# Kernel tuning notes

Measured on AMD Instinct MI355X. Metric: run time of the kernel, lower is better.

## Reference

```python
import jax, jax.numpy as jnp
import numpy as np

H = 8  # heads
EPS = 1e-5


def adaln(x, t, W, b):
    # AdaLayerNorm: emb = Linear(t); scale, shift = chunk(emb, 2, dim=-1)
    emb = t @ W + b                      # [B,1,2*D]
    scale, shift = jnp.split(emb, 2, axis=-1)
    mu = jnp.mean(x, axis=-1, keepdims=True)
    var = jnp.var(x, axis=-1, keepdims=True)
    xn = (x - mu) / jnp.sqrt(var + EPS)  # elementwise_affine=False
    return xn * (1.0 + scale) + shift


def attention(x, ctx, Wq, Wk, Wv, Wo, bo):
    B, N, D = x.shape
    d = D // H
    q = (x @ Wq).reshape(B, N, H, d).transpose(0, 2, 1, 3)          # [B,H,N,d]
    k = (ctx @ Wk).reshape(B, ctx.shape[1], H, d).transpose(0, 2, 1, 3)
    v = (ctx @ Wv).reshape(B, ctx.shape[1], H, d).transpose(0, 2, 1, 3)
    sim = jnp.einsum('bhid,bhjd->bhij', q, k) * (d ** -0.5)
    attn = jax.nn.softmax(sim, axis=-1)
    out = jnp.einsum('bhij,bhjd->bhid', attn, v)
    out = out.transpose(0, 2, 1, 3).reshape(B, N, D)
    return out @ Wo + bo


def geglu_ff(x, W1, b1, W2, b2):
    u, g = jnp.split(x @ W1 + b1, 2, axis=-1)
    return (u * jax.nn.gelu(g, approximate=False)) @ W2 + b2


def setup_inputs() -> dict:
    key = jax.random.key(0)
    ks = jax.random.split(key, 16)
    D = 512
    s = 0.02
    inp = {
        'x': jax.random.normal(ks[0], (2, 2048, D), jnp.float32),
        't': jax.random.normal(ks[1], (2, 1, D), jnp.float32),
        'cond': jax.random.normal(ks[2], (2, 1024, D), jnp.float32),
        'n1_w': jax.random.normal(ks[3], (D, 2 * D), jnp.float32) * s,
        'n1_b': jnp.zeros((2 * D,), jnp.float32),
        'n2_w': jax.random.normal(ks[4], (D, 2 * D), jnp.float32) * s,
        'n2_b': jnp.zeros((2 * D,), jnp.float32),
        'n4_w': jax.random.normal(ks[5], (D, 2 * D), jnp.float32) * s,
        'n4_b': jnp.zeros((2 * D,), jnp.float32),
        'a1_q': jax.random.normal(ks[6], (D, D), jnp.float32) * s,
        'a1_k': jax.random.normal(ks[7], (D, D), jnp.float32) * s,
        'a1_v': jax.random.normal(ks[8], (D, D), jnp.float32) * s,
        'a1_o': jax.random.normal(ks[9], (D, D), jnp.float32) * s,
        'a1_ob': jnp.zeros((D,), jnp.float32),
        'a2_q': jax.random.normal(ks[10], (D, D), jnp.float32) * s,
        'a2_k': jax.random.normal(ks[11], (D, D), jnp.float32) * s,
        'a2_v': jax.random.normal(ks[12], (D, D), jnp.float32) * s,
        'a2_o': jax.random.normal(ks[13], (D, D), jnp.float32) * s,
        'a2_ob': jnp.zeros((D,), jnp.float32),
        'ff_w1': jax.random.normal(ks[14], (D, 8 * D), jnp.float32) * s,
        'ff_b1': jnp.zeros((8 * D,), jnp.float32),
        'ff_w2': jax.random.normal(ks[15], (4 * D, D), jnp.float32) * s,
        'ff_b2': jnp.zeros((D,), jnp.float32),
    }
    return inp


def reference(x, t, cond, n1_w, n1_b, n2_w, n2_b, n4_w, n4_b,
              a1_q, a1_k, a1_v, a1_o, a1_ob,
              a2_q, a2_k, a2_v, a2_o, a2_ob,
              ff_w1, ff_b1, ff_w2, ff_b2):
    # BasicTransformerBlock, is_deform=False, withT=False, inference (dropout/droppath = identity, LayerScale = identity since init_values=0)
    h = adaln(x, t, n1_w, n1_b)
    x = attention(h, h, a1_q, a1_k, a1_v, a1_o, a1_ob) + x
    h = adaln(x, t, n2_w, n2_b)
    x = attention(h, cond, a2_q, a2_k, a2_v, a2_o, a2_ob) + x
    h = adaln(x, t, n4_w, n4_b)
    x = geglu_ff(h, ff_w1, ff_b1, ff_w2, ff_b2) + x
    return x
```

## Files before the change

kernel.cpp:

```cpp
#include <hip/hip_runtime.h>
#include <math.h>

#define D_MODEL 512
#define NHEADS  8
#define DHEAD   64

typedef __bf16  bf16x2 __attribute__((ext_vector_type(2)));
typedef __bf16  bf16x4 __attribute__((ext_vector_type(4)));
typedef __bf16  bf16x8 __attribute__((ext_vector_type(8)));
typedef float   f32x4  __attribute__((ext_vector_type(4)));

#define QSCALE 0.18033688f
#define DEFER_THR 11.5416f

__device__ __forceinline__ void gload16(const __bf16* g, __bf16* l) {
    __builtin_amdgcn_global_load_lds(
        (const __attribute__((address_space(1))) unsigned int*)g,
        (__attribute__((address_space(3))) unsigned int*)l, 16, 0, 0);
}

__device__ __forceinline__ void transpose_tile(
        const float* __restrict__ src, __bf16* __restrict__ dst,
        int K, int N, int k0, int n0) {
    __shared__ float t[64][65];
    int tid = threadIdx.x;
    int r = tid >> 6, c = tid & 63;
#pragma unroll
    for (int i = 0; i < 16; ++i)
        t[r + 4 * i][c] = src[(size_t)(k0 + r + 4 * i) * N + n0 + c];
    __syncthreads();
#pragma unroll
    for (int i = 0; i < 16; ++i)
        dst[(size_t)(n0 + r + 4 * i) * K + k0 + c] = (__bf16)t[c][r + 4 * i];
}

struct PrepArgs {
    const float *t, *n1w, *n1b, *n2w, *n2b, *n4w, *n4b;
    float* emb;
    const float* ws[8]; __bf16* wd[8];
    const float *ffw1, *ffw2;
    __bf16 *ff1t, *ff2t;
    const float* cond; __bf16* cbf;
    int B, condN;
};

__global__ __launch_bounds__(256) void prep_kernel(PrepArgs a) {
    int bb = blockIdx.x, tid = threadIdx.x;
    if (bb < 24) {
        int gI = bb * 256 + tid;
        int per = a.B * 2 * D_MODEL;
        if (gI >= 3 * per) return;
        int norm = gI / per;
        int rem  = gI - norm * per;
        int b = rem / (2 * D_MODEL);
        int c = rem % (2 * D_MODEL);
        const float* W  = (norm == 0) ? a.n1w : (norm == 1 ? a.n2w : a.n4w);
        const float* bb_= (norm == 0) ? a.n1b : (norm == 1 ? a.n2b : a.n4b);
        const float* trow = a.t + (size_t)b * D_MODEL;
        float acc = bb_[c];
        for (int k = 0; k < D_MODEL; ++k)
            acc = fmaf(trow[k], W[(size_t)k * (2 * D_MODEL) + c], acc);
        a.emb[gI] = acc;
    } else if (bb < 536) {
        int w = (bb - 24) >> 6, tI = (bb - 24) & 63;
        transpose_tile(a.ws[w], a.wd[w], 512, 512, (tI >> 3) << 6, (tI & 7) << 6);
    } else if (bb < 1048) {
        int tI = bb - 536;
        transpose_tile(a.ffw1, a.ff1t, 512, 4096, (tI & 7) << 6, (tI >> 3) << 6);
    } else if (bb < 1304) {
        int tI = bb - 1048;
        transpose_tile(a.ffw2, a.ff2t, 2048, 512, (tI >> 3) << 6, (tI & 7) << 6);
    } else {
        int i = ((bb - 1304) * 256 + tid) * 4;
        if (i >= a.condN) return;
        float4 v = *(const float4*)(a.cond + i);
        bf16x2 p0, p1;
        p0[0] = (__bf16)v.x; p0[1] = (__bf16)v.y;
        p1[0] = (__bf16)v.z; p1[1] = (__bf16)v.w;
        *(bf16x2*)(a.cbf + i)     = p0;
        *(bf16x2*)(a.cbf + i + 2) = p1;
    }
}

__global__ __launch_bounds__(256) void adaln_apply_kernel(
        const float* __restrict__ x, const float* __restrict__ emb_n,
        __bf16* __restrict__ h, int N) {
    int row = blockIdx.x;
    int b = row / N;
    const float* xr = x + (size_t)row * D_MODEL;
    int tid = threadIdx.x;
    float2 v = *(const float2*)(xr + 2 * tid);
    float s = v.x + v.y, sq = v.x * v.x + v.y * v.y;
#pragma unroll
    for (int off = 32; off; off >>= 1) {
        s  += __shfl_xor(s, off);
        sq += __shfl_xor(sq, off);
    }
    __shared__ float rs[4], rq[4];
    if ((tid & 63) == 0) { rs[tid >> 6] = s; rq[tid >> 6] = sq; }
    __syncthreads();
    float tot  = rs[0] + rs[1] + rs[2] + rs[3];
    float totq = rq[0] + rq[1] + rq[2] + rq[3];
    float mu  = tot * (1.0f / D_MODEL);
    float var = totq * (1.0f / D_MODEL) - mu * mu;
    float inv = rsqrtf(var + 1e-5f);
    const float* er = emb_n + (size_t)b * (2 * D_MODEL);
    float2 sc = *(const float2*)(er + 2 * tid);
    float2 sh = *(const float2*)(er + D_MODEL + 2 * tid);
    bf16x2 o;
    o[0] = (__bf16)((v.x - mu) * inv * (1.0f + sc.x) + sh.x);
    o[1] = (__bf16)((v.y - mu) * inv * (1.0f + sc.y) + sh.y);
    *(bf16x2*)(h + (size_t)row * D_MODEL + 2 * tid) = o;
}

template<int OUT, int WM>
__device__ __forceinline__ void gemm_body(
        const __bf16* __restrict__ A, const __bf16* __restrict__ Bt,
        const float* __restrict__ bias, const float* __restrict__ res,
        void* __restrict__ Cv, int M, int K, int N, int bx, int by,
        __bf16* As, __bf16* Bs) {
    constexpr int MI = WM / 16;
    int tid = threadIdx.x;
    int wave = tid >> 6, lane = tid & 63;
    int wr = wave >> 1, wc = wave & 1;
    int r = lane & 15, g = lane >> 4;
    int rx = r & 7;
    int m0 = by * (2 * WM), n0 = bx << 6;

    int lrow = lane >> 3;
    int lcol = ((lane & 7) ^ lrow) << 3;
    const __bf16* Ag = A  + (size_t)(m0 + (wave << 3) + lrow) * K + lcol;
    const __bf16* Bg = Bt + (size_t)(n0 + (wave << 3) + lrow) * K + lcol;
    __bf16* AsW = As + (size_t)(wave << 3) * 64;
    __bf16* BsW = Bs + (size_t)(wave << 3) * 64;

    f32x4 acc[MI][2];
#pragma unroll
    for (int mi = 0; mi < MI; ++mi)
#pragma unroll
        for (int ni = 0; ni < 2; ++ni) acc[mi][ni] = (f32x4){0.f, 0.f, 0.f, 0.f};

    for (int k0 = 0; k0 < K; k0 += 64) {
        if (k0) __syncthreads();
#pragma unroll
        for (int i = 0; i < MI; ++i)
            gload16(Ag + (size_t)(i * 32) * K + k0, AsW + i * 32 * 64);
#pragma unroll
        for (int j = 0; j < 2; ++j)
            gload16(Bg + (size_t)(j * 32) * K + k0, BsW + j * 32 * 64);
        __syncthreads();
#pragma unroll
        for (int kk = 0; kk < 2; ++kk) {
            int cs = ((((kk << 2) + g) ^ rx) << 3);
            bf16x8 af[MI], bf_[2];
#pragma unroll
            for (int mi = 0; mi < MI; ++mi)
                af[mi] = *(const bf16x8*)&As[(size_t)(wr * WM + (mi << 4) + r) * 64 + cs];
#pragma unroll
            for (int ni = 0; ni < 2; ++ni)
                bf_[ni] = *(const bf16x8*)&Bs[(size_t)((wc << 5) + (ni << 4) + r) * 64 + cs];
#pragma unroll
            for (int mi = 0; mi < MI; ++mi)
#pragma unroll
                for (int ni = 0; ni < 2; ++ni)
                    acc[mi][ni] = __builtin_amdgcn_mfma_f32_16x16x32_bf16(
                        af[mi], bf_[ni], acc[mi][ni], 0, 0, 0);
        }
    }

#pragma unroll
    for (int mi = 0; mi < MI; ++mi) {
#pragma unroll
        for (int ni = 0; ni < 2; ++ni) {
            int col = n0 + (wc << 5) + (ni << 4) + r;
            float scl = (OUT == 2 && col < 512) ? QSCALE : 1.0f;
#pragma unroll
            for (int rg = 0; rg < 4; ++rg) {
                int row = m0 + wr * WM + (mi << 4) + (g << 2) + rg;
                if (OUT == 1) {
                    float v = acc[mi][ni][rg] + bias[col] + res[(size_t)row * N + col];
                    ((float*)Cv)[(size_t)row * N + col] = v;
                } else {
                    ((__bf16*)Cv)[(size_t)row * N + col] = (__bf16)(acc[mi][ni][rg] * scl);
                }
            }
        }
    }
}

template<int OUT, int WM>
__global__ __launch_bounds__(256) void gemm_bf16_kernel(
        const __bf16* __restrict__ A, const __bf16* __restrict__ Bt,
        const float* __restrict__ bias, const float* __restrict__ res,
        void* __restrict__ Cv, int M, int K, int N) {
    __shared__ __attribute__((aligned(16))) __bf16 As[2 * WM * 64];
    __shared__ __attribute__((aligned(16))) __bf16 Bs[64 * 64];
    gemm_body<OUT, WM>(A, Bt, bias, res, Cv, M, K, N, blockIdx.x, blockIdx.y, As, Bs);
}

__global__ __launch_bounds__(256) void gemm_dual_kernel(
        const __bf16* A0, const __bf16* B0, __bf16* C0, int M0,
        const __bf16* A1, const __bf16* B1, __bf16* C1, int M1) {
    __shared__ __attribute__((aligned(16))) __bf16 As[64 * 64];
    __shared__ __attribute__((aligned(16))) __bf16 Bs[64 * 64];
    int nb0 = 8 * (M0 >> 6);
    if ((int)blockIdx.x < nb0) {
        gemm_body<2, 32>(A0, B0, nullptr, nullptr, C0, M0, 512, 512,
                         blockIdx.x & 7, blockIdx.x >> 3, As, Bs);
    } else {
        int id = blockIdx.x - nb0;
        gemm_body<0, 32>(A1, B1, nullptr, nullptr, C1, M1, 512, 1024,
                         id & 15, id >> 4, As, Bs);
    }
}

__global__ __launch_bounds__(256) void gemm_geglu_bf16_kernel(
        const __bf16* __restrict__ A, const __bf16* __restrict__ W1t,
        const float* __restrict__ b1, __bf16* __restrict__ gg, int M, int K) {
    const int NOUT = 4 * D_MODEL;
    __shared__ __attribute__((aligned(16))) __bf16 AsL[128 * 64];
    __shared__ __attribute__((aligned(16))) __bf16 BuL[64 * 64];
    __shared__ __attribute__((aligned(16))) __bf16 BgL[64 * 64];
    int tid = threadIdx.x;
    int wave = tid >> 6, lane = tid & 63;
    int wr = wave >> 1, wc = wave & 1;
    int r = lane & 15, g = lane >> 4;
    int rx = r & 7;
    int m0 = blockIdx.y << 7, n0 = blockIdx.x << 6;

    int lrow = lane >> 3;
    int lcol = ((lane & 7) ^ lrow) << 3;
    const __bf16* Ag = A   + (size_t)(m0 + (wave << 3) + lrow) * K + lcol;
    const __bf16* Ug = W1t + (size_t)(n0 + (wave << 3) + lrow) * K + lcol;
    const __bf16* Gg = W1t + (size_t)(NOUT + n0 + (wave << 3) + lrow) * K + lcol;
    __bf16* AsW = AsL + (size_t)(wave << 3) * 64;
    __bf16* BuW = BuL + (size_t)(wave << 3) * 64;
    __bf16* BgW = BgL + (size_t)(wave << 3) * 64;

    f32x4 accu[4][2], accg[4][2];
#pragma unroll
    for (int mi = 0; mi < 4; ++mi)
#pragma unroll
        for (int ni = 0; ni < 2; ++ni) {
            accu[mi][ni] = (f32x4){0.f, 0.f, 0.f, 0.f};
            accg[mi][ni] = (f32x4){0.f, 0.f, 0.f, 0.f};
        }

    for (int k0 = 0; k0 < K; k0 += 64) {
        if (k0) __syncthreads();
#pragma unroll
        for (int i = 0; i < 4; ++i)
            gload16(Ag + (size_t)(i * 32) * K + k0, AsW + i * 32 * 64);
#pragma unroll
        for (int j = 0; j < 2; ++j) {
            gload16(Ug + (size_t)(j * 32) * K + k0, BuW + j * 32 * 64);
            gload16(Gg + (size_t)(j * 32) * K + k0, BgW + j * 32 * 64);
        }
        __syncthreads();
#pragma unroll
        for (int kk = 0; kk < 2; ++kk) {
            int cs = ((((kk << 2) + g) ^ rx) << 3);
            bf16x8 af[4], bu[2], bg[2];
#pragma unroll
            for (int mi = 0; mi < 4; ++mi)
                af[mi] = *(const bf16x8*)&AsL[(size_t)((wr << 6) + (mi << 4) + r) * 64 + cs];
#pragma unroll
            for (int ni = 0; ni < 2; ++ni) {
                bu[ni] = *(const bf16x8*)&BuL[(size_t)((wc << 5) + (ni << 4) + r) * 64 + cs];
                bg[ni] = *(const bf16x8*)&BgL[(size_t)((wc << 5) + (ni << 4) + r) * 64 + cs];
            }
#pragma unroll
            for (int mi = 0; mi < 4; ++mi)
#pragma unroll
                for (int ni = 0; ni < 2; ++ni) {
                    accu[mi][ni] = __builtin_amdgcn_mfma_f32_16x16x32_bf16(
                        af[mi], bu[ni], accu[mi][ni], 0, 0, 0);
                    accg[mi][ni] = __builtin_amdgcn_mfma_f32_16x16x32_bf16(
                        af[mi], bg[ni], accg[mi][ni], 0, 0, 0);
                }
        }
    }

#pragma unroll
    for (int mi = 0; mi < 4; ++mi) {
#pragma unroll
        for (int ni = 0; ni < 2; ++ni) {
            int col = n0 + (wc << 5) + (ni << 4) + r;
            float bu_ = b1[col], bg_ = b1[NOUT + col];
#pragma unroll
            for (int rg = 0; rg < 4; ++rg) {
                int row = m0 + (wr << 6) + (mi << 4) + (g << 2) + rg;
                float u  = accu[mi][ni][rg] + bu_;
                float gv = accg[mi][ni][rg] + bg_;
                float ge = 0.5f * gv * (1.0f + erff(gv * 0.70710678118654752f));
                gg[(size_t)row * NOUT + col] = (__bf16)(u * ge);
            }
        }
    }
}

__global__ __launch_bounds__(256) void attn_mfma_kernel(
        const __bf16* __restrict__ q, const __bf16* __restrict__ k,
        const __bf16* __restrict__ v, __bf16* __restrict__ o,
        int Nq, int Nk, int sq, int skv) {
    __shared__ __attribute__((aligned(16))) __bf16 Ks[2][4096];
    __shared__ __attribute__((aligned(16))) __bf16 Vt[2][4096];
    __shared__ __attribute__((aligned(16))) __bf16 Pl[4][1024];

    int tid = threadIdx.x;
    int w = tid >> 6, lane = tid & 63;
    int r = lane & 15, g = lane >> 4;
    int rx = r & 7;

    int nqb = Nq >> 6;
    int qb = blockIdx.x % nqb;
    int hh = (blockIdx.x / nqb) % NHEADS;
    int b  = blockIdx.x / (nqb * NHEADS);

    const __bf16* qp = q + ((size_t)(b * Nq + (qb << 6) + (w << 4) + r)) * sq
                         + hh * DHEAD + (g << 3);
    bf16x8 qf0 = *(const bf16x8*)qp;
    bf16x8 qf1 = *(const bf16x8*)(qp + 32);

    int krow = tid >> 2, kp_ = tid & 3;
    int va = tid & 31, vbb = tid >> 5;
    size_t kvbase = (size_t)b * Nk * skv + (size_t)hh * DHEAD;
    const __bf16* kp = k + kvbase + (size_t)krow * skv + (kp_ << 4);
    const __bf16* vp = v + kvbase + (size_t)(2 * va) * skv + (vbb << 3);
    int kwo0 = krow * 64 + ((((kp_ << 1) | 0) ^ (krow & 7)) << 3);
    int kwo1 = krow * 64 + ((((kp_ << 1) | 1) ^ (krow & 7)) << 3);
    int vwb  = vbb * 512 + ((va & 3) << 1);

    f32x4 oacc[4];
#pragma unroll
    for (int dt = 0; dt < 4; ++dt) oacc[dt] = (f32x4){0.f, 0.f, 0.f, 0.f};
    float m = -1e30f, l = 0.f;
    f32x4 saccA[4], saccB[4];
    bf16x8 kr0, kr1, vr0, vr1;
    bf16x8 vf[2][4], pa[2];

    auto LOADREG = [&](int t) {
        const __bf16* kp2 = kp + (size_t)t * 64 * skv;
        const __bf16* vp2 = vp + (size_t)t * 64 * skv;
        kr0 = *(const bf16x8*)kp2; kr1 = *(const bf16x8*)(kp2 + 8);
        vr0 = *(const bf16x8*)vp2; vr1 = *(const bf16x8*)(vp2 + skv);
    };
    auto STAGEW = [&](int buf) {
        *(bf16x8*)&Ks[buf][kwo0] = kr0;
        *(bf16x8*)&Ks[buf][kwo1] = kr1;
#pragma unroll
        for (int j = 0; j < 8; ++j) {
            bf16x2 pr; pr[0] = vr0[j]; pr[1] = vr1[j];
            *(bf16x2*)&Vt[buf][vwb + j * 64 + (((va >> 2) ^ j) << 3)] = pr;
        }
    };
    auto QKT = [&](f32x4 (&sacc)[4], int buf) {
#pragma unroll
        for (int nt = 0; nt < 4; ++nt) sacc[nt] = (f32x4){0.f, 0.f, 0.f, 0.f};
        __builtin_amdgcn_s_setprio(1);
#pragma unroll
        for (int nt = 0; nt < 4; ++nt) {
            bf16x8 kf0 = *(const bf16x8*)&Ks[buf][((nt << 4) + r) * 64 + ((g ^ rx) << 3)];
            bf16x8 kf1 = *(const bf16x8*)&Ks[buf][((nt << 4) + r) * 64 + (((g + 4) ^ rx) << 3)];
            sacc[nt] = __builtin_amdgcn_mfma_f32_16x16x32_bf16(kf0, qf0, sacc[nt], 0, 0, 0);
            sacc[nt] = __builtin_amdgcn_mfma_f32_16x16x32_bf16(kf1, qf1, sacc[nt], 0, 0, 0);
        }
        __builtin_amdgcn_s_setprio(0);
    };
    auto SMAX = [&](f32x4 (&sacc)[4]) {
        float mx = sacc[0][0];
#pragma unroll
        for (int nt = 0; nt < 4; ++nt)
#pragma unroll
            for (int rg = 0; rg < 4; ++rg) mx = fmaxf(mx, sacc[nt][rg]);
        mx = fmaxf(mx, __shfl_xor(mx, 16));
        mx = fmaxf(mx, __shfl_xor(mx, 32));
        if (!__all(mx <= m + DEFER_THR)) {
            float mn = fmaxf(m, mx);
            float al = exp2f(m - mn);
            m = mn; l *= al;
#pragma unroll
            for (int dt = 0; dt < 4; ++dt)
#pragma unroll
                for (int rg = 0; rg < 4; ++rg) oacc[dt][rg] *= al;
        }
        float sum = 0.f;
#pragma unroll
        for (int nt = 0; nt < 4; ++nt) {
            bf16x4 pk;
#pragma unroll
            for (int rg = 0; rg < 4; ++rg) {
                float p = exp2f(sacc[nt][rg] - m);
                sum += p;
                pk[rg] = (__bf16)p;
            }
            *(bf16x4*)&Pl[w][r * 64 + ((((nt << 1) | (g >> 1)) ^ rx) << 3) + ((g & 1) << 2)] = pk;
        }
        sum += __shfl_xor(sum, 16);
        sum += __shfl_xor(sum, 32);
        l += sum;
    };
    auto VFLOAD = [&](int buf) {
#pragma unroll
        for (int kh = 0; kh < 2; ++kh) {
            pa[kh] = *(const bf16x8*)&Pl[w][r * 64 + ((((kh << 2) + g) ^ rx) << 3)];
#pragma unroll
            for (int dt = 0; dt < 4; ++dt)
                vf[kh][dt] = *(const bf16x8*)&Vt[buf][((dt << 4) + r) * 64
                                                      + ((((kh << 2) + g) ^ rx) << 3)];
        }
    };
    auto PVOP = [&]() {
        __builtin_amdgcn_s_setprio(1);
#pragma unroll
        for (int kh = 0; kh < 2; ++kh)
#pragma unroll
            for (int dt = 0; dt < 4; ++dt)
                oacc[dt] = __builtin_amdgcn_mfma_f32_16x16x32_bf16(
                    vf[kh][dt], pa[kh], oacc[dt], 0, 0, 0);
        __builtin_amdgcn_s_setprio(0);
    };

    int ntiles = Nk >> 6;
    LOADREG(0);
    STAGEW(0);
    LOADREG(1);
    __syncthreads();
    QKT(saccA, 0);

    for (int t = 0; t + 1 < ntiles; t += 2) {
        STAGEW(1);
        if (t + 2 < ntiles) LOADREG(t + 2);
        SMAX(saccA);
        VFLOAD(0);
        __syncthreads();
        QKT(saccB, 1);
        PVOP();
        if (t + 2 < ntiles) {
            STAGEW(0);
            if (t + 3 < ntiles) LOADREG(t + 3);
        }
        SMAX(saccB);
        VFLOAD(1);
        __syncthreads();
        if (t + 2 < ntiles) QKT(saccA, 0);
        PVOP();
    }

    float inv = 1.0f / l;
    __bf16* ob = o + ((size_t)(b * Nq + (qb << 6) + (w << 4) + r)) * D_MODEL + hh * DHEAD;
#pragma unroll
    for (int dt = 0; dt < 4; ++dt) {
        bf16x4 ov;
#pragma unroll
        for (int rg = 0; rg < 4; ++rg) ov[rg] = (__bf16)(oacc[dt][rg] * inv);
        *(bf16x4*)&ob[(dt << 4) + (g << 2)] = ov;
    }
}

extern "C" void kernel_launch(void* const* d_in, const int* in_sizes, int n_in,
                              void* d_out, int out_size, void* d_ws, size_t ws_size,
                              hipStream_t stream) {
    const float* x    = (const float*)d_in[0];
    const float* t    = (const float*)d_in[1];
    const float* cond = (const float*)d_in[2];
    const float* n1_w = (const float*)d_in[3];
    const float* n1_b = (const float*)d_in[4];
    const float* n2_w = (const float*)d_in[5];
    const float* n2_b = (const float*)d_in[6];
    const float* n4_w = (const float*)d_in[7];
    const float* n4_b = (const float*)d_in[8];
    const float* a1_q = (const float*)d_in[9];
    const float* a1_k = (const float*)d_in[10];
    const float* a1_v = (const float*)d_in[11];
    const float* a1_o = (const float*)d_in[12];
    const float* a1_ob= (const float*)d_in[13];
    const float* a2_q = (const float*)d_in[14];
    const float* a2_k = (const float*)d_in[15];
    const float* a2_v = (const float*)d_in[16];
    const float* a2_o = (const float*)d_in[17];
    const float* a2_ob= (const float*)d_in[18];
    const float* ff_w1= (const float*)d_in[19];
    const float* ff_b1= (const float*)d_in[20];
    const float* ff_w2= (const float*)d_in[21];
    const float* ff_b2= (const float*)d_in[22];
    float* out = (float*)d_out;

    const int B  = in_sizes[1] / D_MODEL;
    const int N  = in_sizes[0] / (B * D_MODEL);
    const int Nc = in_sizes[2] / (B * D_MODEL);
    const int R  = B * N;
    const int Rc = B * Nc;

    char* Wb = (char*)d_ws;
    float* emb   = (float*)Wb;
    __bf16* r1   = (__bf16*)(Wb + 32768);
    __bf16* qkv  = r1;
    __bf16* q2   = r1;
    __bf16* kv2  = r1 + (size_t)R * 512;
    __bf16* gg   = r1;
    __bf16* h_bf = (__bf16*)(Wb + 32768 + 16777216);
    __bf16* c_bf = (__bf16*)(Wb + 32768 + 16777216 + 4194304);
    __bf16* wts  = (__bf16*)(Wb + 32768 + 16777216 + 4194304 + 2097152);
    __bf16* a1_qt = wts;
    __bf16* a1_ot = wts + 3 * 262144;
    __bf16* a2_qt = wts + 4 * 262144;
    __bf16* a2_kt = wts + 5 * 262144;
    __bf16* a2_ot = wts + 7 * 262144;
    __bf16* ff1t  = wts + 8 * 262144;
    __bf16* ff2t  = ff1t + 2097152;

    dim3 blk(256);

    PrepArgs pa;
    pa.t = t; pa.n1w = n1_w; pa.n1b = n1_b; pa.n2w = n2_w; pa.n2b = n2_b;
    pa.n4w = n4_w; pa.n4b = n4_b; pa.emb = emb;
    pa.ws[0] = a1_q; pa.ws[1] = a1_k; pa.ws[2] = a1_v; pa.ws[3] = a1_o;
    pa.ws[4] = a2_q; pa.ws[5] = a2_k; pa.ws[6] = a2_v; pa.ws[7] = a2_o;
    pa.wd[0] = a1_qt; pa.wd[1] = wts + 262144; pa.wd[2] = wts + 2 * 262144; pa.wd[3] = a1_ot;
    pa.wd[4] = a2_qt; pa.wd[5] = a2_kt; pa.wd[6] = wts + 6 * 262144; pa.wd[7] = a2_ot;
    pa.ffw1 = ff_w1; pa.ffw2 = ff_w2; pa.ff1t = ff1t; pa.ff2t = ff2t;
    pa.cond = cond; pa.cbf = c_bf; pa.B = B; pa.condN = Rc * D_MODEL;
    prep_kernel<<<dim3(1304 + (Rc * D_MODEL) / 1024), blk, 0, stream>>>(pa);

    adaln_apply_kernel<<<dim3(R), blk, 0, stream>>>(x, emb, h_bf, N);
    gemm_bf16_kernel<2, 64><<<dim3(24, R / 128), blk, 0, stream>>>(
        h_bf, a1_qt, nullptr, nullptr, qkv, R, 512, 1536);
    attn_mfma_kernel<<<dim3(B * NHEADS * (N / 64)), blk, 0, stream>>>(
        qkv, qkv + 512, qkv + 1024, h_bf, N, N, 1536, 1536);
    gemm_bf16_kernel<1, 32><<<dim3(8, R / 64), blk, 0, stream>>>(
        h_bf, a1_ot, a1_ob, x, out, R, 512, 512);

    adaln_apply_kernel<<<dim3(R), blk, 0, stream>>>(
        out, emb + (size_t)B * 2 * D_MODEL, h_bf, N);
    gemm_dual_kernel<<<dim3(8 * (R / 64) + 16 * (Rc / 64)), blk, 0, stream>>>(
        h_bf, a2_qt, q2, R, c_bf, a2_kt, kv2, Rc);
    attn_mfma_kernel<<<dim3(B * NHEADS * (N / 64)), blk, 0, stream>>>(
        q2, kv2, kv2 + 512, h_bf, N, Nc, 512, 1024);
    gemm_bf16_kernel<1, 32><<<dim3(8, R / 64), blk, 0, stream>>>(
        h_bf, a2_ot, a2_ob, out, out, R, 512, 512);

    adaln_apply_kernel<<<dim3(R), blk, 0, stream>>>(
        out, emb + (size_t)2 * B * 2 * D_MODEL, h_bf, N);
    gemm_geglu_bf16_kernel<<<dim3(32, R / 128), blk, 0, stream>>>(
        h_bf, ff1t, ff_b1, gg, R, 512);
    gemm_bf16_kernel<1, 32><<<dim3(8, R / 64), blk, 0, stream>>>(
        gg, ff2t, ff_b2, out, out, R, 2048, 512);
}
```

Before: 218.4 us.

## Load K fragments straight from global into registers, dropping K LDS staging

```diff
diff --git a/kernel.cpp b/kernel.cpp
--- a/kernel.cpp
+++ b/kernel.cpp
@@ -303,7 +303,6 @@
         const __bf16* __restrict__ q, const __bf16* __restrict__ k,
         const __bf16* __restrict__ v, __bf16* __restrict__ o,
         int Nq, int Nk, int sq, int skv) {
-    __shared__ __attribute__((aligned(16))) __bf16 Ks[2][4096];
     __shared__ __attribute__((aligned(16))) __bf16 Vt[2][4096];
     __shared__ __attribute__((aligned(16))) __bf16 Pl[4][1024];
 
@@ -322,52 +321,53 @@
     bf16x8 qf0 = *(const bf16x8*)qp;
     bf16x8 qf1 = *(const bf16x8*)(qp + 32);
 
-    int krow = tid >> 2, kp_ = tid & 3;
+    size_t kvbase = (size_t)b * Nk * skv + (size_t)hh * DHEAD;
+    const __bf16* kfb = k + kvbase + (size_t)r * skv + (g << 3);
     int va = tid & 31, vbb = tid >> 5;
-    size_t kvbase = (size_t)b * Nk * skv + (size_t)hh * DHEAD;
-    const __bf16* kp = k + kvbase + (size_t)krow * skv + (kp_ << 4);
     const __bf16* vp = v + kvbase + (size_t)(2 * va) * skv + (vbb << 3);
-    int kwo0 = krow * 64 + ((((kp_ << 1) | 0) ^ (krow & 7)) << 3);
-    int kwo1 = krow * 64 + ((((kp_ << 1) | 1) ^ (krow & 7)) << 3);
-    int vwb  = vbb * 512 + ((va & 3) << 1);
+    int vwb = vbb * 512 + ((va & 3) << 1);
 
     f32x4 oacc[4];
 #pragma unroll
     for (int dt = 0; dt < 4; ++dt) oacc[dt] = (f32x4){0.f, 0.f, 0.f, 0.f};
     float m = -1e30f, l = 0.f;
-    f32x4 saccA[4], saccB[4];
-    bf16x8 kr0, kr1, vr0, vr1;
+    bf16x8 kfA[4][2], kfB[4][2];
+    bf16x8 vr0, vr1;
     bf16x8 vf[2][4], pa[2];
-
-    auto LOADREG = [&](int t) {
-        const __bf16* kp2 = kp + (size_t)t * 64 * skv;
+    f32x4 sacc[4];
+
+    auto KLOAD = [&](bf16x8 (&kf)[4][2], int t) {
+        const __bf16* kp2 = kfb + (size_t)t * 64 * skv;
+#pragma unroll
+        for (int nt = 0; nt < 4; ++nt)
+#pragma unroll
+            for (int kh = 0; kh < 2; ++kh)
+                kf[nt][kh] = *(const bf16x8*)(kp2 + (size_t)(nt * 16) * skv + kh * 32);
+    };
+    auto VLOAD = [&](int t) {
         const __bf16* vp2 = vp + (size_t)t * 64 * skv;
-        kr0 = *(const bf16x8*)kp2; kr1 = *(const bf16x8*)(kp2 + 8);
-        vr0 = *(const bf16x8*)vp2; vr1 = *(const bf16x8*)(vp2 + skv);
+        vr0 = *(const bf16x8*)vp2;
+        vr1 = *(const bf16x8*)(vp2 + skv);
     };
     auto STAGEW = [&](int buf) {
-        *(bf16x8*)&Ks[buf][kwo0] = kr0;
-        *(bf16x8*)&Ks[buf][kwo1] = kr1;
 #pragma unroll
         for (int j = 0; j < 8; ++j) {
             bf16x2 pr; pr[0] = vr0[j]; pr[1] = vr1[j];
             *(bf16x2*)&Vt[buf][vwb + j * 64 + (((va >> 2) ^ j) << 3)] = pr;
         }
     };
-    auto QKT = [&](f32x4 (&sacc)[4], int buf) {
+    auto QKT = [&](bf16x8 (&kf)[4][2]) {
 #pragma unroll
         for (int nt = 0; nt < 4; ++nt) sacc[nt] = (f32x4){0.f, 0.f, 0.f, 0.f};
         __builtin_amdgcn_s_setprio(1);
 #pragma unroll
         for (int nt = 0; nt < 4; ++nt) {
-            bf16x8 kf0 = *(const bf16x8*)&Ks[buf][((nt << 4) + r) * 64 + ((g ^ rx) << 3)];
-            bf16x8 kf1 = *(const bf16x8*)&Ks[buf][((nt << 4) + r) * 64 + (((g + 4) ^ rx) << 3)];
-            sacc[nt] = __builtin_amdgcn_mfma_f32_16x16x32_bf16(kf0, qf0, sacc[nt], 0, 0, 0);
-            sacc[nt] = __builtin_amdgcn_mfma_f32_16x16x32_bf16(kf1, qf1, sacc[nt], 0, 0, 0);
+            sacc[nt] = __builtin_amdgcn_mfma_f32_16x16x32_bf16(kf[nt][0], qf0, sacc[nt], 0, 0, 0);
+            sacc[nt] = __builtin_amdgcn_mfma_f32_16x16x32_bf16(kf[nt][1], qf1, sacc[nt], 0, 0, 0);
         }
         __builtin_amdgcn_s_setprio(0);
     };
-    auto SMAX = [&](f32x4 (&sacc)[4]) {
+    auto SMAX = [&]() {
         float mx = sacc[0][0];
 #pragma unroll
         for (int nt = 0; nt < 4; ++nt)
@@ -396,8 +396,6 @@
             }
             *(bf16x4*)&Pl[w][r * 64 + ((((nt << 1) | (g >> 1)) ^ rx) << 3) + ((g & 1) << 2)] = pk;
         }
-        sum += __shfl_xor(sum, 16);
-        sum += __shfl_xor(sum, 32);
         l += sum;
     };
     auto VFLOAD = [&](int buf) {
@@ -422,31 +420,33 @@
     };
 
     int ntiles = Nk >> 6;
-    LOADREG(0);
+    VLOAD(0);
     STAGEW(0);
-    LOADREG(1);
+    KLOAD(kfA, 0);
+    KLOAD(kfB, 1);
+    VLOAD(1);
     __syncthreads();
-    QKT(saccA, 0);
-
-    for (int t = 0; t + 1 < ntiles; t += 2) {
-        STAGEW(1);
-        if (t + 2 < ntiles) LOADREG(t + 2);
-        SMAX(saccA);
+
+    for (int t = 0; t < ntiles; t += 2) {
+        QKT(kfA);
+        if (t + 1 < ntiles) STAGEW(1);
+        if (t + 2 < ntiles) { KLOAD(kfA, t + 2); VLOAD(t + 2); }
+        SMAX();
         VFLOAD(0);
+        PVOP();
         __syncthreads();
-        QKT(saccB, 1);
+        if (t + 1 >= ntiles) break;
+        QKT(kfB);
+        if (t + 2 < ntiles) STAGEW(0);
+        if (t + 3 < ntiles) { KLOAD(kfB, t + 3); VLOAD(t + 3); }
+        SMAX();
+        VFLOAD(1);
         PVOP();
-        if (t + 2 < ntiles) {
-            STAGEW(0);
-            if (t + 3 < ntiles) LOADREG(t + 3);
-        }
-        SMAX(saccB);
-        VFLOAD(1);
         __syncthreads();
-        if (t + 2 < ntiles) QKT(saccA, 0);
-        PVOP();
-    }
-
+    }
+
+    l += __shfl_xor(l, 16);
+    l += __shfl_xor(l, 32);
     float inv = 1.0f / l;
     __bf16* ob = o + ((size_t)(b * Nq + (qb << 6) + (w << 4) + r)) * D_MODEL + hh * DHEAD;
 #pragma unroll
```

After: 265.5 us. +21.6%, slower.

## Double attention query tile to 128 rows with 8 waves sharing K/V staging

Applied to the files above, without the earlier changes.

```diff
diff --git a/kernel.cpp b/kernel.cpp
--- a/kernel.cpp
+++ b/kernel.cpp
@@ -299,31 +299,33 @@
     }
 }
 
-__global__ __launch_bounds__(256) void attn_mfma_kernel(
+__global__ __launch_bounds__(512) void attn_mfma_kernel(
         const __bf16* __restrict__ q, const __bf16* __restrict__ k,
         const __bf16* __restrict__ v, __bf16* __restrict__ o,
         int Nq, int Nk, int sq, int skv) {
     __shared__ __attribute__((aligned(16))) __bf16 Ks[2][4096];
     __shared__ __attribute__((aligned(16))) __bf16 Vt[2][4096];
-    __shared__ __attribute__((aligned(16))) __bf16 Pl[4][1024];
+    __shared__ __attribute__((aligned(16))) __bf16 Pl[8][1024];
 
     int tid = threadIdx.x;
     int w = tid >> 6, lane = tid & 63;
     int r = lane & 15, g = lane >> 4;
     int rx = r & 7;
 
-    int nqb = Nq >> 6;
+    int nqb = Nq >> 7;
     int qb = blockIdx.x % nqb;
     int hh = (blockIdx.x / nqb) % NHEADS;
     int b  = blockIdx.x / (nqb * NHEADS);
 
-    const __bf16* qp = q + ((size_t)(b * Nq + (qb << 6) + (w << 4) + r)) * sq
+    const __bf16* qp = q + ((size_t)(b * Nq + (qb << 7) + (w << 4) + r)) * sq
                          + hh * DHEAD + (g << 3);
     bf16x8 qf0 = *(const bf16x8*)qp;
     bf16x8 qf1 = *(const bf16x8*)(qp + 32);
 
-    int krow = tid >> 2, kp_ = tid & 3;
-    int va = tid & 31, vbb = tid >> 5;
+    bool isK = (tid >= 256);
+    int sidx = tid & 255;
+    int krow = sidx >> 2, kp_ = sidx & 3;
+    int va = sidx & 31, vbb = sidx >> 5;
     size_t kvbase = (size_t)b * Nk * skv + (size_t)hh * DHEAD;
     const __bf16* kp = k + kvbase + (size_t)krow * skv + (kp_ << 4);
     const __bf16* vp = v + kvbase + (size_t)(2 * va) * skv + (vbb << 3);
@@ -336,22 +338,28 @@
     for (int dt = 0; dt < 4; ++dt) oacc[dt] = (f32x4){0.f, 0.f, 0.f, 0.f};
     float m = -1e30f, l = 0.f;
     f32x4 saccA[4], saccB[4];
-    bf16x8 kr0, kr1, vr0, vr1;
+    bf16x8 sr0, sr1;
     bf16x8 vf[2][4], pa[2];
 
     auto LOADREG = [&](int t) {
-        const __bf16* kp2 = kp + (size_t)t * 64 * skv;
-        const __bf16* vp2 = vp + (size_t)t * 64 * skv;
-        kr0 = *(const bf16x8*)kp2; kr1 = *(const bf16x8*)(kp2 + 8);
-        vr0 = *(const bf16x8*)vp2; vr1 = *(const bf16x8*)(vp2 + skv);
+        if (isK) {
+            const __bf16* kp2 = kp + (size_t)t * 64 * skv;
+            sr0 = *(const bf16x8*)kp2; sr1 = *(const bf16x8*)(kp2 + 8);
+        } else {
+            const __bf16* vp2 = vp + (size_t)t * 64 * skv;
+            sr0 = *(const bf16x8*)vp2; sr1 = *(const bf16x8*)(vp2 + skv);
+        }
     };
     auto STAGEW = [&](int buf) {
-        *(bf16x8*)&Ks[buf][kwo0] = kr0;
-        *(bf16x8*)&Ks[buf][kwo1] = kr1;
-#pragma unroll
-        for (int j = 0; j < 8; ++j) {
-            bf16x2 pr; pr[0] = vr0[j]; pr[1] = vr1[j];
-            *(bf16x2*)&Vt[buf][vwb + j * 64 + (((va >> 2) ^ j) << 3)] = pr;
+        if (isK) {
+            *(bf16x8*)&Ks[buf][kwo0] = sr0;
+            *(bf16x8*)&Ks[buf][kwo1] = sr1;
+        } else {
+#pragma unroll
+            for (int j = 0; j < 8; ++j) {
+                bf16x2 pr; pr[0] = sr0[j]; pr[1] = sr1[j];
+                *(bf16x2*)&Vt[buf][vwb + j * 64 + (((va >> 2) ^ j) << 3)] = pr;
+            }
         }
     };
     auto QKT = [&](f32x4 (&sacc)[4], int buf) {
@@ -396,8 +404,6 @@
             }
             *(bf16x4*)&Pl[w][r * 64 + ((((nt << 1) | (g >> 1)) ^ rx) << 3) + ((g & 1) << 2)] = pk;
         }
-        sum += __shfl_xor(sum, 16);
-        sum += __shfl_xor(sum, 32);
         l += sum;
     };
     auto VFLOAD = [&](int buf) {
@@ -447,8 +453,10 @@
         PVOP();
     }
 
+    l += __shfl_xor(l, 16);
+    l += __shfl_xor(l, 32);
     float inv = 1.0f / l;
-    __bf16* ob = o + ((size_t)(b * Nq + (qb << 6) + (w << 4) + r)) * D_MODEL + hh * DHEAD;
+    __bf16* ob = o + ((size_t)(b * Nq + (qb << 7) + (w << 4) + r)) * D_MODEL + hh * DHEAD;
 #pragma unroll
     for (int dt = 0; dt < 4; ++dt) {
         bf16x4 ov;
@@ -526,7 +534,7 @@
     adaln_apply_kernel<<<dim3(R), blk, 0, stream>>>(x, emb, h_bf, N);
     gemm_bf16_kernel<2, 64><<<dim3(24, R / 128), blk, 0, stream>>>(
         h_bf, a1_qt, nullptr, nullptr, qkv, R, 512, 1536);
-    attn_mfma_kernel<<<dim3(B * NHEADS * (N / 64)), blk, 0, stream>>>(
+    attn_mfma_kernel<<<dim3(B * NHEADS * (N / 128)), dim3(512), 0, stream>>>(
         qkv, qkv + 512, qkv + 1024, h_bf, N, N, 1536, 1536);
     gemm_bf16_kernel<1, 32><<<dim3(8, R / 64), blk, 0, stream>>>(
         h_bf, a1_ot, a1_ob, x, out, R, 512, 512);
@@ -535,7 +543,7 @@
         out, emb + (size_t)B * 2 * D_MODEL, h_bf, N);
     gemm_dual_kernel<<<dim3(8 * (R / 64) + 16 * (Rc / 64)), blk, 0, stream>>>(
         h_bf, a2_qt, q2, R, c_bf, a2_kt, kv2, Rc);
-    attn_mfma_kernel<<<dim3(B * NHEADS * (N / 64)), blk, 0, stream>>>(
+    attn_mfma_kernel<<<dim3(B * NHEADS * (N / 128)), dim3(512), 0, stream>>>(
         q2, kv2, kv2 + 512, h_bf, N, Nc, 512, 1024);
     gemm_bf16_kernel<1, 32><<<dim3(8, R / 64), blk, 0, stream>>>(
         h_bf, a2_ot, a2_ob, out, out, R, 512, 512);
```

After: 211.3 us, median of 2. 3.2% less time.

## Switch attention to 32x32x16 MFMA with 128-query blocks and XCD-aware block mapping

Applied to the files above, without the earlier changes.

```diff
diff --git a/kernel.cpp b/kernel.cpp
--- a/kernel.cpp
+++ b/kernel.cpp
@@ -9,6 +9,7 @@
 typedef __bf16  bf16x4 __attribute__((ext_vector_type(4)));
 typedef __bf16  bf16x8 __attribute__((ext_vector_type(8)));
 typedef float   f32x4  __attribute__((ext_vector_type(4)));
+typedef float   f32x16 __attribute__((ext_vector_type(16)));
 
 #define QSCALE 0.18033688f
 #define DEFER_THR 11.5416f
@@ -305,22 +306,29 @@
         int Nq, int Nk, int sq, int skv) {
     __shared__ __attribute__((aligned(16))) __bf16 Ks[2][4096];
     __shared__ __attribute__((aligned(16))) __bf16 Vt[2][4096];
-    __shared__ __attribute__((aligned(16))) __bf16 Pl[4][1024];
+    __shared__ __attribute__((aligned(16))) __bf16 Pl[4][2048];
 
     int tid = threadIdx.x;
     int w = tid >> 6, lane = tid & 63;
-    int r = lane & 15, g = lane >> 4;
-    int rx = r & 7;
-
-    int nqb = Nq >> 6;
-    int qb = blockIdx.x % nqb;
-    int hh = (blockIdx.x / nqb) % NHEADS;
-    int b  = blockIdx.x / (nqb * NHEADS);
-
-    const __bf16* qp = q + ((size_t)(b * Nq + (qb << 6) + (w << 4) + r)) * sq
-                         + hh * DHEAD + (g << 3);
-    bf16x8 qf0 = *(const bf16x8*)qp;
-    bf16x8 qf1 = *(const bf16x8*)(qp + 32);
+    int c = lane & 31;
+    int hg = lane >> 5;
+    int cx = c & 7;
+
+    int nwg = gridDim.x;
+    int cpx = nwg >> 3;
+    int bid = (int)blockIdx.x;
+    int lb  = (bid & 7) * cpx + (bid >> 3);
+
+    int nqb = Nq >> 7;
+    int qb = lb % nqb;
+    int hh = (lb / nqb) % NHEADS;
+    int b  = lb / (nqb * NHEADS);
+
+    const __bf16* qp = q + ((size_t)(b * Nq + (qb << 7) + (w << 5) + c)) * sq
+                         + hh * DHEAD + (hg << 3);
+    bf16x8 qf[4];
+#pragma unroll
+    for (int ks = 0; ks < 4; ++ks) qf[ks] = *(const bf16x8*)(qp + ks * 16);
 
     int krow = tid >> 2, kp_ = tid & 3;
     int va = tid & 31, vbb = tid >> 5;
@@ -331,13 +339,15 @@
     int kwo1 = krow * 64 + ((((kp_ << 1) | 1) ^ (krow & 7)) << 3);
     int vwb  = vbb * 512 + ((va & 3) << 1);
 
-    f32x4 oacc[4];
-#pragma unroll
-    for (int dt = 0; dt < 4; ++dt) oacc[dt] = (f32x4){0.f, 0.f, 0.f, 0.f};
+    f32x16 oacc[2];
+#pragma unroll
+    for (int db = 0; db < 2; ++db)
+#pragma unroll
+        for (int rg = 0; rg < 16; ++rg) oacc[db][rg] = 0.f;
     float m = -1e30f, l = 0.f;
-    f32x4 saccA[4], saccB[4];
+    f32x16 saccA[2], saccB[2];
     bf16x8 kr0, kr1, vr0, vr1;
-    bf16x8 vf[2][4], pa[2];
+    bf16x8 vf[2][4], pb[4];
 
     auto LOADREG = [&](int t) {
         const __bf16* kp2 = kp + (size_t)t * 64 * skv;
@@ -354,70 +364,80 @@
             *(bf16x2*)&Vt[buf][vwb + j * 64 + (((va >> 2) ^ j) << 3)] = pr;
         }
     };
-    auto QKT = [&](f32x4 (&sacc)[4], int buf) {
-#pragma unroll
-        for (int nt = 0; nt < 4; ++nt) sacc[nt] = (f32x4){0.f, 0.f, 0.f, 0.f};
+    auto QKT = [&](f32x16 (&sacc)[2], int buf) {
+#pragma unroll
+        for (int kb = 0; kb < 2; ++kb)
+#pragma unroll
+            for (int rg = 0; rg < 16; ++rg) sacc[kb][rg] = 0.f;
         __builtin_amdgcn_s_setprio(1);
 #pragma unroll
-        for (int nt = 0; nt < 4; ++nt) {
-            bf16x8 kf0 = *(const bf16x8*)&Ks[buf][((nt << 4) + r) * 64 + ((g ^ rx) << 3)];
-            bf16x8 kf1 = *(const bf16x8*)&Ks[buf][((nt << 4) + r) * 64 + (((g + 4) ^ rx) << 3)];
-            sacc[nt] = __builtin_amdgcn_mfma_f32_16x16x32_bf16(kf0, qf0, sacc[nt], 0, 0, 0);
-            sacc[nt] = __builtin_amdgcn_mfma_f32_16x16x32_bf16(kf1, qf1, sacc[nt], 0, 0, 0);
+        for (int kb = 0; kb < 2; ++kb) {
+#pragma unroll
+            for (int ks = 0; ks < 4; ++ks) {
+                int row = (kb << 5) + c;
+                bf16x8 kf = *(const bf16x8*)&Ks[buf][row * 64
+                                + ((((ks << 1) + hg) ^ cx) << 3)];
+                sacc[kb] = __builtin_amdgcn_mfma_f32_32x32x16_bf16(
+                    kf, qf[ks], sacc[kb], 0, 0, 0);
+            }
         }
         __builtin_amdgcn_s_setprio(0);
     };
-    auto SMAX = [&](f32x4 (&sacc)[4]) {
+    auto SMAX = [&](f32x16 (&sacc)[2]) {
         float mx = sacc[0][0];
 #pragma unroll
-        for (int nt = 0; nt < 4; ++nt)
-#pragma unroll
-            for (int rg = 0; rg < 4; ++rg) mx = fmaxf(mx, sacc[nt][rg]);
-        mx = fmaxf(mx, __shfl_xor(mx, 16));
+        for (int kb = 0; kb < 2; ++kb)
+#pragma unroll
+            for (int rg = 0; rg < 16; ++rg) mx = fmaxf(mx, sacc[kb][rg]);
         mx = fmaxf(mx, __shfl_xor(mx, 32));
         if (!__all(mx <= m + DEFER_THR)) {
             float mn = fmaxf(m, mx);
             float al = exp2f(m - mn);
             m = mn; l *= al;
 #pragma unroll
-            for (int dt = 0; dt < 4; ++dt)
-#pragma unroll
-                for (int rg = 0; rg < 4; ++rg) oacc[dt][rg] *= al;
+            for (int db = 0; db < 2; ++db)
+#pragma unroll
+                for (int rg = 0; rg < 16; ++rg) oacc[db][rg] *= al;
         }
         float sum = 0.f;
 #pragma unroll
-        for (int nt = 0; nt < 4; ++nt) {
-            bf16x4 pk;
-#pragma unroll
-            for (int rg = 0; rg < 4; ++rg) {
-                float p = exp2f(sacc[nt][rg] - m);
-                sum += p;
-                pk[rg] = (__bf16)p;
+        for (int kb = 0; kb < 2; ++kb) {
+#pragma unroll
+            for (int rg4 = 0; rg4 < 4; ++rg4) {
+                bf16x4 pk;
+#pragma unroll
+                for (int rr = 0; rr < 4; ++rr) {
+                    float p = exp2f(sacc[kb][(rg4 << 2) + rr] - m);
+                    sum += p;
+                    pk[rr] = (__bf16)p;
+                }
+                int slot = (kb << 2) + rg4;
+                *(bf16x4*)&Pl[w][c * 64 + ((slot ^ cx) << 3) + (hg << 2)] = pk;
             }
-            *(bf16x4*)&Pl[w][r * 64 + ((((nt << 1) | (g >> 1)) ^ rx) << 3) + ((g & 1) << 2)] = pk;
-        }
-        sum += __shfl_xor(sum, 16);
-        sum += __shfl_xor(sum, 32);
+        }
         l += sum;
     };
     auto VFLOAD = [&](int buf) {
 #pragma unroll
-        for (int kh = 0; kh < 2; ++kh) {
-            pa[kh] = *(const bf16x8*)&Pl[w][r * 64 + ((((kh << 2) + g) ^ rx) << 3)];
-#pragma unroll
-            for (int dt = 0; dt < 4; ++dt)
-                vf[kh][dt] = *(const bf16x8*)&Vt[buf][((dt << 4) + r) * 64
-                                                      + ((((kh << 2) + g) ^ rx) << 3)];
-        }
+        for (int ks = 0; ks < 4; ++ks)
+            pb[ks] = *(const bf16x8*)&Pl[w][c * 64 + ((((ks << 1) + hg) ^ cx) << 3)];
+#pragma unroll
+        for (int db = 0; db < 2; ++db)
+#pragma unroll
+            for (int ks = 0; ks < 4; ++ks) {
+                int row = (db << 5) + c;
+                vf[db][ks] = *(const bf16x8*)&Vt[buf][row * 64
+                                + ((((ks << 1) + hg) ^ cx) << 3)];
+            }
     };
     auto PVOP = [&]() {
         __builtin_amdgcn_s_setprio(1);
 #pragma unroll
-        for (int kh = 0; kh < 2; ++kh)
-#pragma unroll
-            for (int dt = 0; dt < 4; ++dt)
-                oacc[dt] = __builtin_amdgcn_mfma_f32_16x16x32_bf16(
-                    vf[kh][dt], pa[kh], oacc[dt], 0, 0, 0);
+        for (int db = 0; db < 2; ++db)
+#pragma unroll
+            for (int ks = 0; ks < 4; ++ks)
+                oacc[db] = __builtin_amdgcn_mfma_f32_32x32x16_bf16(
+                    vf[db][ks], pb[ks], oacc[db], 0, 0, 0);
         __builtin_amdgcn_s_setprio(0);
     };
 
@@ -447,14 +467,19 @@
         PVOP();
     }
 
+    l += __shfl_xor(l, 32);
     float inv = 1.0f / l;
-    __bf16* ob = o + ((size_t)(b * Nq + (qb << 6) + (w << 4) + r)) * D_MODEL + hh * DHEAD;
-#pragma unroll
-    for (int dt = 0; dt < 4; ++dt) {
-        bf16x4 ov;
-#pragma unroll
-        for (int rg = 0; rg < 4; ++rg) ov[rg] = (__bf16)(oacc[dt][rg] * inv);
-        *(bf16x4*)&ob[(dt << 4) + (g << 2)] = ov;
+    __bf16* ob = o + ((size_t)(b * Nq + (qb << 7) + (w << 5) + c)) * D_MODEL + hh * DHEAD;
+#pragma unroll
+    for (int db = 0; db < 2; ++db) {
+#pragma unroll
+        for (int rg4 = 0; rg4 < 4; ++rg4) {
+            bf16x4 ov;
+#pragma unroll
+            for (int rr = 0; rr < 4; ++rr)
+                ov[rr] = (__bf16)(oacc[db][(rg4 << 2) + rr] * inv);
+            *(bf16x4*)&ob[(db << 5) + (rg4 << 3) + (hg << 2)] = ov;
+        }
     }
 }
 
@@ -526,7 +551,7 @@
     adaln_apply_kernel<<<dim3(R), blk, 0, stream>>>(x, emb, h_bf, N);
     gemm_bf16_kernel<2, 64><<<dim3(24, R / 128), blk, 0, stream>>>(
         h_bf, a1_qt, nullptr, nullptr, qkv, R, 512, 1536);
-    attn_mfma_kernel<<<dim3(B * NHEADS * (N / 64)), blk, 0, stream>>>(
+    attn_mfma_kernel<<<dim3(B * NHEADS * (N / 128)), dim3(256), 0, stream>>>(
         qkv, qkv + 512, qkv + 1024, h_bf, N, N, 1536, 1536);
     gemm_bf16_kernel<1, 32><<<dim3(8, R / 64), blk, 0, stream>>>(
         h_bf, a1_ot, a1_ob, x, out, R, 512, 512);
@@ -535,7 +560,7 @@
         out, emb + (size_t)B * 2 * D_MODEL, h_bf, N);
     gemm_dual_kernel<<<dim3(8 * (R / 64) + 16 * (Rc / 64)), blk, 0, stream>>>(
         h_bf, a2_qt, q2, R, c_bf, a2_kt, kv2, Rc);
-    attn_mfma_kernel<<<dim3(B * NHEADS * (N / 64)), blk, 0, stream>>>(
+    attn_mfma_kernel<<<dim3(B * NHEADS * (N / 128)), dim3(256), 0, stream>>>(
         q2, kv2, kv2 + 512, h_bf, N, Nc, 512, 1024);
     gemm_bf16_kernel<1, 32><<<dim3(8, R / 64), blk, 0, stream>>>(
         h_bf, a2_ot, a2_ob, out, out, R, 512, 512);
```

Measured after the change: 230.0 us. 1.05x slower.
